# Performance work log

Measured on AMD Instinct MI355X. Metric: run time of the kernel, lower is better.

## Reference

```python
import jax, jax.numpy as jnp
import numpy as np

BETA = 0.9       # snn.Leaky(beta=0.9)
THRESH = 1.0     # snntorch default threshold, reset_mechanism='subtract'


def setup_inputs() -> dict:
    key = jax.random.key(0)
    ks = jax.random.split(key, 7)
    B = 16384
    return {
        "x":  jax.random.normal(ks[0], (B, 1700), dtype=jnp.float32),
        "W1": jax.random.normal(ks[1], (64, 1700), dtype=jnp.float32) * 0.02,
        "b1": jax.random.normal(ks[2], (64,), dtype=jnp.float32) * 0.02,
        "W2": jax.random.normal(ks[3], (32, 64), dtype=jnp.float32) * 0.1,
        "b2": jax.random.normal(ks[4], (32,), dtype=jnp.float32) * 0.1,
        "W3": jax.random.normal(ks[5], (2, 32), dtype=jnp.float32) * 0.1,
        "b3": jax.random.normal(ks[6], (2,), dtype=jnp.float32) * 0.1,
        "num_steps": 20,
    }


def _lif_step(mem, cur):
    # snntorch Leaky: reset (subtract) based on previous mem crossing threshold,
    # then leaky integration of the new input current.
    reset = (mem > THRESH).astype(mem.dtype)
    return BETA * mem + cur - reset * THRESH


def reference(x, W1, b1, W2, b2, W3, b3, num_steps):
    B = x.shape[0]
    # Dropout is identity in eval mode; x is constant across steps, so cur1 is
    # loop-invariant and computed once (same math as the original loop).
    cur1 = x @ W1.T + b1                         # [B, 64]

    def step(carry, _):
        mem1, mem2 = carry
        mem1 = _lif_step(mem1, cur1)             # [B, 64]
        cur2 = mem1 @ W2.T + b2                  # [B, 32]
        mem2 = _lif_step(mem2, cur2)             # [B, 32]
        return (mem1, mem2), None

    init = (jnp.zeros((B, 64), x.dtype), jnp.zeros((B, 32), x.dtype))
    (mem1, mem2), _ = jax.lax.scan(step, init, None, length=num_steps)
    return mem2 @ W3.T + b3                      # [B, 2]
```

## Files before the change

kernel.cpp:

```cpp
#include <hip/hip_runtime.h>
#include <hip/hip_bf16.h>

typedef float f32x4 __attribute__((ext_vector_type(4)));
typedef short bf16x8 __attribute__((ext_vector_type(8)));

#define MFMA16 __builtin_amdgcn_mfma_f32_16x16x32_bf16

static constexpr int KDIM = 1700;
static constexpr int NKT  = 54;
static constexpr float BETA = 0.9f;
static constexpr float THRESH = 1.0f;

__device__ __forceinline__ void split_bf(float f, short& hi, short& lo) {
    __hip_bfloat16 h = __float2bfloat16(f);
    float r = f - __bfloat162float(h);
    __hip_bfloat16 l = __float2bfloat16(r);
    hi = (short)__builtin_bit_cast(unsigned short, h);
    lo = (short)__builtin_bit_cast(unsigned short, l);
}

__device__ __forceinline__ void split8(f32x4 a, f32x4 b, bf16x8& hi, bf16x8& lo) {
    #pragma unroll
    for (int i = 0; i < 4; ++i) { short h, l; split_bf(a[i], h, l); hi[i] = h; lo[i] = l; }
    #pragma unroll
    for (int i = 0; i < 4; ++i) { short h, l; split_bf(b[i], h, l); hi[4 + i] = h; lo[4 + i] = l; }
}

__global__ void w1_relayout(const float* __restrict__ W1,
                            short* __restrict__ WTh, short* __restrict__ WTl) {
    const int g    = blockIdx.x * 256 + threadIdx.x;
    const int kt   = g >> 8;
    const int nt   = (g >> 6) & 3;
    const int lane = g & 63;
    const int n    = nt * 16 + (lane & 15);
    const int kb   = kt * 32 + (lane >> 4) * 8;
    bf16x8 vh, vl;
    #pragma unroll
    for (int i = 0; i < 8; ++i) {
        const int k = kb + i;
        const float v = (k < KDIM) ? W1[n * KDIM + k] : 0.f;
        short h, l; split_bf(v, h, l);
        vh[i] = h; vl[i] = l;
    }
    *(bf16x8*)(WTh + (size_t)g * 8) = vh;
    *(bf16x8*)(WTl + (size_t)g * 8) = vl;
}

__global__ __launch_bounds__(256, 2) void gemm1(
    const float* __restrict__ x,
    const short* __restrict__ WTh, const short* __restrict__ WTl,
    const float* __restrict__ b1, float* __restrict__ cur1)
{
    __shared__ float red[4][32][68];
    const int tid = threadIdx.x;
    const int wid = tid >> 6;
    const int lane = tid & 63;
    const int l15 = lane & 15;
    const int g4  = lane >> 4;
    const int kg  = g4 * 8;
    const int rowBase = blockIdx.x * 32;

    const int t0  = wid * 13 + (wid < 2 ? wid : 2);
    const int t1  = t0 + 14 - (wid >> 1);
    const int t1e = (wid == 3) ? 53 : t1;

    f32x4 acc[2][4] = {};
    const float* xr0 = x + (size_t)(rowBase + l15) * KDIM + kg;
    const float* xr1 = xr0 + (size_t)16 * KDIM;

    f32x4 p00 = *(const f32x4*)(xr0 + t0 * 32);
    f32x4 p01 = *(const f32x4*)(xr0 + t0 * 32 + 4);
    f32x4 p10 = *(const f32x4*)(xr1 + t0 * 32);
    f32x4 p11 = *(const f32x4*)(xr1 + t0 * 32 + 4);

    for (int t = t0; t < t1e; ++t) {
        f32x4 a00 = p00, a01 = p01, a10 = p10, a11 = p11;
        if (t + 1 < t1e) {
            p00 = *(const f32x4*)(xr0 + (t + 1) * 32);
            p01 = *(const f32x4*)(xr0 + (t + 1) * 32 + 4);
            p10 = *(const f32x4*)(xr1 + (t + 1) * 32);
            p11 = *(const f32x4*)(xr1 + (t + 1) * 32 + 4);
        }
        const short* wb = WTh + (size_t)t * 2048 + lane * 8;
        const short* wl = WTl + (size_t)t * 2048 + lane * 8;
        bf16x8 bh[4], bl[4];
        #pragma unroll
        for (int nt = 0; nt < 4; ++nt) {
            bh[nt] = *(const bf16x8*)(wb + nt * 512);
            bl[nt] = *(const bf16x8*)(wl + nt * 512);
        }
        bf16x8 ah0, al0, ah1, al1;
        split8(a00, a01, ah0, al0);
        split8(a10, a11, ah1, al1);
        #pragma unroll
        for (int nt = 0; nt < 4; ++nt) {
            acc[0][nt] = MFMA16(ah0, bh[nt], acc[0][nt], 0, 0, 0);
            acc[0][nt] = MFMA16(al0, bh[nt], acc[0][nt], 0, 0, 0);
            acc[0][nt] = MFMA16(ah0, bl[nt], acc[0][nt], 0, 0, 0);
            acc[1][nt] = MFMA16(ah1, bh[nt], acc[1][nt], 0, 0, 0);
            acc[1][nt] = MFMA16(al1, bh[nt], acc[1][nt], 0, 0, 0);
            acc[1][nt] = MFMA16(ah1, bl[nt], acc[1][nt], 0, 0, 0);
        }
    }
    if (wid == 3) {
        f32x4 a00 = {0,0,0,0}, a01 = {0,0,0,0}, a10 = {0,0,0,0}, a11 = {0,0,0,0};
        if (g4 == 0) {
            a00 = *(const f32x4*)(xr0 + 53 * 32);
            a10 = *(const f32x4*)(xr1 + 53 * 32);
        }
        const short* wb = WTh + (size_t)53 * 2048 + lane * 8;
        const short* wl = WTl + (size_t)53 * 2048 + lane * 8;
        bf16x8 bh[4], bl[4];
        #pragma unroll
        for (int nt = 0; nt < 4; ++nt) {
            bh[nt] = *(const bf16x8*)(wb + nt * 512);
            bl[nt] = *(const bf16x8*)(wl + nt * 512);
        }
        bf16x8 ah0, al0, ah1, al1;
        split8(a00, a01, ah0, al0);
        split8(a10, a11, ah1, al1);
        #pragma unroll
        for (int nt = 0; nt < 4; ++nt) {
            acc[0][nt] = MFMA16(ah0, bh[nt], acc[0][nt], 0, 0, 0);
            acc[0][nt] = MFMA16(al0, bh[nt], acc[0][nt], 0, 0, 0);
            acc[0][nt] = MFMA16(ah0, bl[nt], acc[0][nt], 0, 0, 0);
            acc[1][nt] = MFMA16(ah1, bh[nt], acc[1][nt], 0, 0, 0);
            acc[1][nt] = MFMA16(al1, bh[nt], acc[1][nt], 0, 0, 0);
            acc[1][nt] = MFMA16(ah1, bl[nt], acc[1][nt], 0, 0, 0);
        }
    }

    #pragma unroll
    for (int mt = 0; mt < 2; ++mt)
        #pragma unroll
        for (int nt = 0; nt < 4; ++nt)
            #pragma unroll
            for (int j = 0; j < 4; ++j)
                red[wid][mt * 16 + g4 * 4 + j][nt * 16 + l15] = acc[mt][nt][j];
    __syncthreads();

    const int rr  = tid >> 3;
    const int seg = tid & 7;
    f32x4 s0 = {0,0,0,0}, s1 = {0,0,0,0};
    #pragma unroll
    for (int p = 0; p < 4; ++p) {
        s0 += *(const f32x4*)&red[p][rr][seg * 8];
        s1 += *(const f32x4*)&red[p][rr][seg * 8 + 4];
    }
    s0 += *(const f32x4*)(b1 + seg * 8);
    s1 += *(const f32x4*)(b1 + seg * 8 + 4);
    float* cp = cur1 + (size_t)(rowBase + rr) * 64 + seg * 8;
    *(f32x4*)cp = s0;
    *(f32x4*)(cp + 4) = s1;
}

__global__ __launch_bounds__(256, 2) void recur(
    const float* __restrict__ cur1, const float* __restrict__ W2,
    const float* __restrict__ b2, const float* __restrict__ W3,
    const float* __restrict__ b3, const int* __restrict__ nsp,
    float* __restrict__ out)
{
    const int tid = threadIdx.x;
    const int wid = tid >> 6;
    const int lane = tid & 63;
    const int l15 = lane & 15;
    const int g4  = lane >> 4;
    const int kg  = g4 * 8;
    const int row = blockIdx.x * 64 + wid * 16 + l15;

    float c1[2][8];
    #pragma unroll
    for (int kt = 0; kt < 2; ++kt) {
        f32x4 u0 = *(const f32x4*)(cur1 + (size_t)row * 64 + kt * 32 + kg);
        f32x4 u1 = *(const f32x4*)(cur1 + (size_t)row * 64 + kt * 32 + kg + 4);
        #pragma unroll
        for (int i = 0; i < 4; ++i) { c1[kt][i] = u0[i]; c1[kt][4 + i] = u1[i]; }
    }

    bf16x8 W2hf[2][2], W2lf[2][2];
    #pragma unroll
    for (int rt = 0; rt < 2; ++rt)
        #pragma unroll
        for (int kt = 0; kt < 2; ++kt) {
            const float* wp = W2 + (rt * 16 + l15) * 64 + kt * 32 + kg;
            split8(*(const f32x4*)wp, *(const f32x4*)(wp + 4), W2hf[rt][kt], W2lf[rt][kt]);
        }

    float b2v[2][4], w3a[2][4], w3b[2][4];
    #pragma unroll
    for (int nt = 0; nt < 2; ++nt)
        #pragma unroll
        for (int j = 0; j < 4; ++j) {
            const int o = nt * 16 + g4 * 4 + j;
            b2v[nt][j] = b2[o];
            w3a[nt][j] = W3[o];
            w3b[nt][j] = W3[32 + o];
        }

    float m1[2][8] = {};
    float m2[2][4] = {};
    const int ns = nsp[0];
    for (int s = 0; s < ns; ++s) {
        bf16x8 mh[2], ml[2];
        #pragma unroll
        for (int kt = 0; kt < 2; ++kt)
            #pragma unroll
            for (int i = 0; i < 8; ++i) {
                float m = m1[kt][i];
                float rr = (m > THRESH) ? THRESH : 0.f;
                m = __builtin_fmaf(BETA, m, c1[kt][i] - rr);
                m1[kt][i] = m;
                short h, l; split_bf(m, h, l);
                mh[kt][i] = h; ml[kt][i] = l;
            }
        f32x4 a2[2][2] = {};
        #pragma unroll
        for (int rt = 0; rt < 2; ++rt)
            #pragma unroll
            for (int kt = 0; kt < 2; ++kt) {
                a2[rt][kt] = MFMA16(W2hf[rt][kt], mh[kt], a2[rt][kt], 0, 0, 0);
                a2[rt][kt] = MFMA16(W2lf[rt][kt], mh[kt], a2[rt][kt], 0, 0, 0);
                a2[rt][kt] = MFMA16(W2hf[rt][kt], ml[kt], a2[rt][kt], 0, 0, 0);
            }
        #pragma unroll
        for (int nt = 0; nt < 2; ++nt) {
            f32x4 c2 = a2[nt][0] + a2[nt][1];
            #pragma unroll
            for (int j = 0; j < 4; ++j) {
                float m = m2[nt][j];
                float rr = (m > THRESH) ? THRESH : 0.f;
                m2[nt][j] = __builtin_fmaf(BETA, m, c2[j] + b2v[nt][j] - rr);
            }
        }
    }

    float p0 = 0.f, p1 = 0.f;
    #pragma unroll
    for (int nt = 0; nt < 2; ++nt)
        #pragma unroll
        for (int j = 0; j < 4; ++j) {
            p0 = __builtin_fmaf(m2[nt][j], w3a[nt][j], p0);
            p1 = __builtin_fmaf(m2[nt][j], w3b[nt][j], p1);
        }
    p0 += __shfl_xor(p0, 16); p0 += __shfl_xor(p0, 32);
    p1 += __shfl_xor(p1, 16); p1 += __shfl_xor(p1, 32);
    if (lane < 16) {
        out[(size_t)row * 2 + 0] = p0 + b3[0];
        out[(size_t)row * 2 + 1] = p1 + b3[1];
    }
}

extern "C" void kernel_launch(void* const* d_in, const int* in_sizes, int n_in,
                              void* d_out, int out_size, void* d_ws, size_t ws_size,
                              hipStream_t stream) {
    const float* x  = (const float*)d_in[0];
    const float* W1 = (const float*)d_in[1];
    const float* b1 = (const float*)d_in[2];
    const float* W2 = (const float*)d_in[3];
    const float* b2 = (const float*)d_in[4];
    const float* W3 = (const float*)d_in[5];
    const float* b3 = (const float*)d_in[6];
    const int*   ns = (const int*)d_in[7];
    float* o = (float*)d_out;

    const int B = in_sizes[0] / KDIM;
    float* cur1 = (float*)d_ws;
    short* WTh  = (short*)((char*)d_ws + (size_t)B * 64 * 4);
    short* WTl  = WTh + (size_t)NKT * 2048;

    w1_relayout<<<NKT, 256, 0, stream>>>(W1, WTh, WTl);
    gemm1<<<B / 32, 256, 0, stream>>>(x, WTh, WTl, b1, cur1);
    recur<<<B / 64, 256, 0, stream>>>(cur1, W2, b2, W3, b3, ns, o);
}
```

Before: 44.51 us.

## Share W1 tiles via LDS with async global-to-LDS loads and 64-row blocks

Each gemm1 block now covers 64 rows instead of 32. The four waves split into two row halves times two K halves, and they stage the W1 hi/lo bf16 planes into double-buffered LDS with global_load_lds. Each wave then reads B fragments from LDS instead of global memory, which removes per-wave redundant weight loads and halves the reduction partners. The costs are a block-wide barrier on every K step, one block per CU from the launch bounds, and half as many blocks.

```diff
diff --git a/kernel.cpp b/kernel.cpp
--- a/kernel.cpp
+++ b/kernel.cpp
@@ -8,6 +8,7 @@
 
 static constexpr int KDIM = 1700;
 static constexpr int NKT  = 54;
+static constexpr int HTILES = 27;
 static constexpr float BETA = 0.9f;
 static constexpr float THRESH = 1.0f;
 
@@ -46,89 +47,93 @@
     *(bf16x8*)(WTl + (size_t)g * 8) = vl;
 }
 
-__global__ __launch_bounds__(256, 2) void gemm1(
+__device__ __forceinline__ void gll16(const short* src, const short* lds_dst) {
+    __builtin_amdgcn_global_load_lds(
+        (const __attribute__((address_space(1))) unsigned int*)src,
+        (__attribute__((address_space(3))) unsigned int*)lds_dst, 16, 0, 0);
+}
+
+__global__ __launch_bounds__(256, 1) void gemm1(
     const float* __restrict__ x,
     const short* __restrict__ WTh, const short* __restrict__ WTl,
     const float* __restrict__ b1, float* __restrict__ cur1)
 {
-    __shared__ float red[4][32][68];
-    const int tid = threadIdx.x;
-    const int wid = tid >> 6;
+    __shared__ __align__(1024) char smem[2 * 64 * 68 * 4];
+    short* ldsW = (short*)smem;
+    float (*red)[64][68] = (float (*)[64][68])smem;
+
+    const int tid  = threadIdx.x;
+    const int wid  = tid >> 6;
     const int lane = tid & 63;
-    const int l15 = lane & 15;
-    const int g4  = lane >> 4;
-    const int kg  = g4 * 8;
-    const int rowBase = blockIdx.x * 32;
-
-    const int t0  = wid * 13 + (wid < 2 ? wid : 2);
-    const int t1  = t0 + 14 - (wid >> 1);
-    const int t1e = (wid == 3) ? 53 : t1;
+    const int l15  = lane & 15;
+    const int g4   = lane >> 4;
+    const int kg   = g4 * 8;
+    const int kh   = wid & 1;
+    const int rh   = wid >> 1;
+    const int rowBase = blockIdx.x * 64;
+
+    const float* xr0 = x + (size_t)(rowBase + rh * 32 + l15) * KDIM + kg;
+    const float* xr1 = xr0 + (size_t)16 * KDIM;
+
+    const short* myPlane = (wid & 1) ? WTl : WTh;
+    const int    myTileOfs = (wid >> 1) ? HTILES : 0;
+
+    auto loadx = [&](int tile, f32x4& a00, f32x4& a01, f32x4& a10, f32x4& a11) {
+        if (tile < 53) {
+            a00 = *(const f32x4*)(xr0 + tile * 32);
+            a01 = *(const f32x4*)(xr0 + tile * 32 + 4);
+            a10 = *(const f32x4*)(xr1 + tile * 32);
+            a11 = *(const f32x4*)(xr1 + tile * 32 + 4);
+        } else {
+            a00 = a01 = a10 = a11 = (f32x4){0, 0, 0, 0};
+            if (g4 == 0) {
+                a00 = *(const f32x4*)(xr0 + 53 * 32);
+                a10 = *(const f32x4*)(xr1 + 53 * 32);
+            }
+        }
+    };
+    auto stage = [&](int buf, int s) {
+        const size_t gofs = (size_t)(myTileOfs + s) * 2048 + lane * 8;
+        const short* dst = ldsW + buf * 8192 + wid * 2048;
+        #pragma unroll
+        for (int i = 0; i < 4; ++i)
+            gll16(myPlane + gofs + i * 512, dst + i * 512);
+    };
+
+    f32x4 a00, a01, a10, a11;
+    loadx(kh * HTILES, a00, a01, a10, a11);
+    stage(0, 0);
+    __syncthreads();
 
     f32x4 acc[2][4] = {};
-    const float* xr0 = x + (size_t)(rowBase + l15) * KDIM + kg;
-    const float* xr1 = xr0 + (size_t)16 * KDIM;
-
-    f32x4 p00 = *(const f32x4*)(xr0 + t0 * 32);
-    f32x4 p01 = *(const f32x4*)(xr0 + t0 * 32 + 4);
-    f32x4 p10 = *(const f32x4*)(xr1 + t0 * 32);
-    f32x4 p11 = *(const f32x4*)(xr1 + t0 * 32 + 4);
-
-    for (int t = t0; t < t1e; ++t) {
-        f32x4 a00 = p00, a01 = p01, a10 = p10, a11 = p11;
-        if (t + 1 < t1e) {
-            p00 = *(const f32x4*)(xr0 + (t + 1) * 32);
-            p01 = *(const f32x4*)(xr0 + (t + 1) * 32 + 4);
-            p10 = *(const f32x4*)(xr1 + (t + 1) * 32);
-            p11 = *(const f32x4*)(xr1 + (t + 1) * 32 + 4);
-        }
-        const short* wb = WTh + (size_t)t * 2048 + lane * 8;
-        const short* wl = WTl + (size_t)t * 2048 + lane * 8;
-        bf16x8 bh[4], bl[4];
-        #pragma unroll
-        for (int nt = 0; nt < 4; ++nt) {
-            bh[nt] = *(const bf16x8*)(wb + nt * 512);
-            bl[nt] = *(const bf16x8*)(wl + nt * 512);
+    f32x4 p00, p01, p10, p11;
+    for (int s = 0; s < HTILES; ++s) {
+        const int buf = s & 1;
+        if (s + 1 < HTILES) {
+            loadx(kh * HTILES + s + 1, p00, p01, p10, p11);
+            stage(buf ^ 1, s + 1);
         }
         bf16x8 ah0, al0, ah1, al1;
         split8(a00, a01, ah0, al0);
         split8(a10, a11, ah1, al1);
+        const short* wb = ldsW + buf * 8192 + kh * 4096;
         #pragma unroll
         for (int nt = 0; nt < 4; ++nt) {
-            acc[0][nt] = MFMA16(ah0, bh[nt], acc[0][nt], 0, 0, 0);
-            acc[0][nt] = MFMA16(al0, bh[nt], acc[0][nt], 0, 0, 0);
-            acc[0][nt] = MFMA16(ah0, bl[nt], acc[0][nt], 0, 0, 0);
-            acc[1][nt] = MFMA16(ah1, bh[nt], acc[1][nt], 0, 0, 0);
-            acc[1][nt] = MFMA16(al1, bh[nt], acc[1][nt], 0, 0, 0);
-            acc[1][nt] = MFMA16(ah1, bl[nt], acc[1][nt], 0, 0, 0);
-        }
-    }
-    if (wid == 3) {
-        f32x4 a00 = {0,0,0,0}, a01 = {0,0,0,0}, a10 = {0,0,0,0}, a11 = {0,0,0,0};
-        if (g4 == 0) {
-            a00 = *(const f32x4*)(xr0 + 53 * 32);
-            a10 = *(const f32x4*)(xr1 + 53 * 32);
-        }
-        const short* wb = WTh + (size_t)53 * 2048 + lane * 8;
-        const short* wl = WTl + (size_t)53 * 2048 + lane * 8;
-        bf16x8 bh[4], bl[4];
-        #pragma unroll
-        for (int nt = 0; nt < 4; ++nt) {
-            bh[nt] = *(const bf16x8*)(wb + nt * 512);
-            bl[nt] = *(const bf16x8*)(wl + nt * 512);
-        }
-        bf16x8 ah0, al0, ah1, al1;
-        split8(a00, a01, ah0, al0);
-        split8(a10, a11, ah1, al1);
-        #pragma unroll
-        for (int nt = 0; nt < 4; ++nt) {
-            acc[0][nt] = MFMA16(ah0, bh[nt], acc[0][nt], 0, 0, 0);
-            acc[0][nt] = MFMA16(al0, bh[nt], acc[0][nt], 0, 0, 0);
-            acc[0][nt] = MFMA16(ah0, bl[nt], acc[0][nt], 0, 0, 0);
-            acc[1][nt] = MFMA16(ah1, bh[nt], acc[1][nt], 0, 0, 0);
-            acc[1][nt] = MFMA16(al1, bh[nt], acc[1][nt], 0, 0, 0);
-            acc[1][nt] = MFMA16(ah1, bl[nt], acc[1][nt], 0, 0, 0);
-        }
-    }
+            bf16x8 bh = *(const bf16x8*)(wb + nt * 512 + lane * 8);
+            bf16x8 bl = *(const bf16x8*)(wb + 2048 + nt * 512 + lane * 8);
+            acc[0][nt] = MFMA16(ah0, bh, acc[0][nt], 0, 0, 0);
+            acc[0][nt] = MFMA16(al0, bh, acc[0][nt], 0, 0, 0);
+            acc[0][nt] = MFMA16(ah0, bl, acc[0][nt], 0, 0, 0);
+            acc[1][nt] = MFMA16(ah1, bh, acc[1][nt], 0, 0, 0);
+            acc[1][nt] = MFMA16(al1, bh, acc[1][nt], 0, 0, 0);
+            acc[1][nt] = MFMA16(ah1, bl, acc[1][nt], 0, 0, 0);
+        }
+        if (s + 1 < HTILES) {
+            __syncthreads();
+            a00 = p00; a01 = p01; a10 = p10; a11 = p11;
+        }
+    }
+    __syncthreads();
 
     #pragma unroll
     for (int mt = 0; mt < 2; ++mt)
@@ -136,22 +141,24 @@
         for (int nt = 0; nt < 4; ++nt)
             #pragma unroll
             for (int j = 0; j < 4; ++j)
-                red[wid][mt * 16 + g4 * 4 + j][nt * 16 + l15] = acc[mt][nt][j];
+                red[kh][rh * 32 + mt * 16 + g4 * 4 + j][nt * 16 + l15] = acc[mt][nt][j];
     __syncthreads();
 
-    const int rr  = tid >> 3;
-    const int seg = tid & 7;
-    f32x4 s0 = {0,0,0,0}, s1 = {0,0,0,0};
-    #pragma unroll
-    for (int p = 0; p < 4; ++p) {
-        s0 += *(const f32x4*)&red[p][rr][seg * 8];
-        s1 += *(const f32x4*)&red[p][rr][seg * 8 + 4];
-    }
-    s0 += *(const f32x4*)(b1 + seg * 8);
-    s1 += *(const f32x4*)(b1 + seg * 8 + 4);
-    float* cp = cur1 + (size_t)(rowBase + rr) * 64 + seg * 8;
-    *(f32x4*)cp = s0;
-    *(f32x4*)(cp + 4) = s1;
+    #pragma unroll
+    for (int it = 0; it < 2; ++it) {
+        const int task = tid + it * 256;
+        const int row = task >> 3;
+        const int seg = task & 7;
+        f32x4 s0 = *(const f32x4*)&red[0][row][seg * 8]
+                 + *(const f32x4*)&red[1][row][seg * 8]
+                 + *(const f32x4*)(b1 + seg * 8);
+        f32x4 s1 = *(const f32x4*)&red[0][row][seg * 8 + 4]
+                 + *(const f32x4*)&red[1][row][seg * 8 + 4]
+                 + *(const f32x4*)(b1 + seg * 8 + 4);
+        float* cp = cur1 + (size_t)(rowBase + row) * 64 + seg * 8;
+        *(f32x4*)cp = s0;
+        *(f32x4*)(cp + 4) = s1;
+    }
 }
 
 __global__ __launch_bounds__(256, 2) void recur(
@@ -269,6 +276,6 @@
     short* WTl  = WTh + (size_t)NKT * 2048;
 
     w1_relayout<<<NKT, 256, 0, stream>>>(W1, WTh, WTl);
-    gemm1<<<B / 32, 256, 0, stream>>>(x, WTh, WTl, b1, cur1);
+    gemm1<<<B / 64, 256, 0, stream>>>(x, WTh, WTl, b1, cur1);
     recur<<<B / 64, 256, 0, stream>>>(cur1, W2, b2, W3, b3, ns, o);
 }
```

New measurement: 53.14 us. 1.19x slower.

## Fuse layer-1 GEMM with LIF recurrence, keeping cur1 in shared memory

Applied to the files above, without the earlier changes.

Merges the gemm1 and recur kernels into one kernel. After the cross-wave reduction, cur1 stays in LDS and is read by two of the four waves, which run the 20-step recurrence, so the cur1 round-trip through global memory and one kernel launch go away. The LIF reset is also rewritten as a select between precomputed (cur - thresh) and cur values, removing a subtract per step. The cost is that half the waves sit idle during the serial recurrence while still holding their registers and LDS.

```diff
diff --git a/kernel.cpp b/kernel.cpp
--- a/kernel.cpp
+++ b/kernel.cpp
@@ -46,10 +46,13 @@
     *(bf16x8*)(WTl + (size_t)g * 8) = vl;
 }
 
-__global__ __launch_bounds__(256, 2) void gemm1(
+__global__ __launch_bounds__(256, 2) void snn_fused(
     const float* __restrict__ x,
     const short* __restrict__ WTh, const short* __restrict__ WTl,
-    const float* __restrict__ b1, float* __restrict__ cur1)
+    const float* __restrict__ b1, const float* __restrict__ W2,
+    const float* __restrict__ b2, const float* __restrict__ W3,
+    const float* __restrict__ b3, const int* __restrict__ nsp,
+    float* __restrict__ out)
 {
     __shared__ float red[4][32][68];
     const int tid = threadIdx.x;
@@ -60,121 +63,115 @@
     const int kg  = g4 * 8;
     const int rowBase = blockIdx.x * 32;
 
-    const int t0  = wid * 13 + (wid < 2 ? wid : 2);
-    const int t1  = t0 + 14 - (wid >> 1);
-    const int t1e = (wid == 3) ? 53 : t1;
-
-    f32x4 acc[2][4] = {};
-    const float* xr0 = x + (size_t)(rowBase + l15) * KDIM + kg;
-    const float* xr1 = xr0 + (size_t)16 * KDIM;
-
-    f32x4 p00 = *(const f32x4*)(xr0 + t0 * 32);
-    f32x4 p01 = *(const f32x4*)(xr0 + t0 * 32 + 4);
-    f32x4 p10 = *(const f32x4*)(xr1 + t0 * 32);
-    f32x4 p11 = *(const f32x4*)(xr1 + t0 * 32 + 4);
-
-    for (int t = t0; t < t1e; ++t) {
-        f32x4 a00 = p00, a01 = p01, a10 = p10, a11 = p11;
-        if (t + 1 < t1e) {
-            p00 = *(const f32x4*)(xr0 + (t + 1) * 32);
-            p01 = *(const f32x4*)(xr0 + (t + 1) * 32 + 4);
-            p10 = *(const f32x4*)(xr1 + (t + 1) * 32);
-            p11 = *(const f32x4*)(xr1 + (t + 1) * 32 + 4);
-        }
-        const short* wb = WTh + (size_t)t * 2048 + lane * 8;
-        const short* wl = WTl + (size_t)t * 2048 + lane * 8;
-        bf16x8 bh[4], bl[4];
-        #pragma unroll
-        for (int nt = 0; nt < 4; ++nt) {
-            bh[nt] = *(const bf16x8*)(wb + nt * 512);
-            bl[nt] = *(const bf16x8*)(wl + nt * 512);
-        }
-        bf16x8 ah0, al0, ah1, al1;
-        split8(a00, a01, ah0, al0);
-        split8(a10, a11, ah1, al1);
-        #pragma unroll
-        for (int nt = 0; nt < 4; ++nt) {
-            acc[0][nt] = MFMA16(ah0, bh[nt], acc[0][nt], 0, 0, 0);
-            acc[0][nt] = MFMA16(al0, bh[nt], acc[0][nt], 0, 0, 0);
-            acc[0][nt] = MFMA16(ah0, bl[nt], acc[0][nt], 0, 0, 0);
-            acc[1][nt] = MFMA16(ah1, bh[nt], acc[1][nt], 0, 0, 0);
-            acc[1][nt] = MFMA16(al1, bh[nt], acc[1][nt], 0, 0, 0);
-            acc[1][nt] = MFMA16(ah1, bl[nt], acc[1][nt], 0, 0, 0);
-        }
-    }
-    if (wid == 3) {
-        f32x4 a00 = {0,0,0,0}, a01 = {0,0,0,0}, a10 = {0,0,0,0}, a11 = {0,0,0,0};
-        if (g4 == 0) {
-            a00 = *(const f32x4*)(xr0 + 53 * 32);
-            a10 = *(const f32x4*)(xr1 + 53 * 32);
-        }
-        const short* wb = WTh + (size_t)53 * 2048 + lane * 8;
-        const short* wl = WTl + (size_t)53 * 2048 + lane * 8;
-        bf16x8 bh[4], bl[4];
-        #pragma unroll
-        for (int nt = 0; nt < 4; ++nt) {
-            bh[nt] = *(const bf16x8*)(wb + nt * 512);
-            bl[nt] = *(const bf16x8*)(wl + nt * 512);
-        }
-        bf16x8 ah0, al0, ah1, al1;
-        split8(a00, a01, ah0, al0);
-        split8(a10, a11, ah1, al1);
-        #pragma unroll
-        for (int nt = 0; nt < 4; ++nt) {
-            acc[0][nt] = MFMA16(ah0, bh[nt], acc[0][nt], 0, 0, 0);
-            acc[0][nt] = MFMA16(al0, bh[nt], acc[0][nt], 0, 0, 0);
-            acc[0][nt] = MFMA16(ah0, bl[nt], acc[0][nt], 0, 0, 0);
-            acc[1][nt] = MFMA16(ah1, bh[nt], acc[1][nt], 0, 0, 0);
-            acc[1][nt] = MFMA16(al1, bh[nt], acc[1][nt], 0, 0, 0);
-            acc[1][nt] = MFMA16(ah1, bl[nt], acc[1][nt], 0, 0, 0);
-        }
-    }
-
-    #pragma unroll
-    for (int mt = 0; mt < 2; ++mt)
-        #pragma unroll
-        for (int nt = 0; nt < 4; ++nt)
-            #pragma unroll
-            for (int j = 0; j < 4; ++j)
-                red[wid][mt * 16 + g4 * 4 + j][nt * 16 + l15] = acc[mt][nt][j];
+    {
+        const int t0  = wid * 13 + (wid < 2 ? wid : 2);
+        const int t1  = t0 + 14 - (wid >> 1);
+        const int t1e = (wid == 3) ? 53 : t1;
+
+        const float* xr0 = x + (size_t)(rowBase + l15) * KDIM + kg;
+        const float* xr1 = xr0 + (size_t)16 * KDIM;
+
+        f32x4 acc[2][4] = {};
+        f32x4 p00 = *(const f32x4*)(xr0 + t0 * 32);
+        f32x4 p01 = *(const f32x4*)(xr0 + t0 * 32 + 4);
+        f32x4 p10 = *(const f32x4*)(xr1 + t0 * 32);
+        f32x4 p11 = *(const f32x4*)(xr1 + t0 * 32 + 4);
+
+        for (int t = t0; t < t1e; ++t) {
+            f32x4 a00 = p00, a01 = p01, a10 = p10, a11 = p11;
+            if (t + 1 < t1e) {
+                p00 = *(const f32x4*)(xr0 + (t + 1) * 32);
+                p01 = *(const f32x4*)(xr0 + (t + 1) * 32 + 4);
+                p10 = *(const f32x4*)(xr1 + (t + 1) * 32);
+                p11 = *(const f32x4*)(xr1 + (t + 1) * 32 + 4);
+            }
+            const short* wb = WTh + (size_t)t * 2048 + lane * 8;
+            const short* wl = WTl + (size_t)t * 2048 + lane * 8;
+            bf16x8 bh[4], bl[4];
+            #pragma unroll
+            for (int nt = 0; nt < 4; ++nt) {
+                bh[nt] = *(const bf16x8*)(wb + nt * 512);
+                bl[nt] = *(const bf16x8*)(wl + nt * 512);
+            }
+            bf16x8 ah0, al0, ah1, al1;
+            split8(a00, a01, ah0, al0);
+            split8(a10, a11, ah1, al1);
+            #pragma unroll
+            for (int nt = 0; nt < 4; ++nt) {
+                acc[0][nt] = MFMA16(ah0, bh[nt], acc[0][nt], 0, 0, 0);
+                acc[0][nt] = MFMA16(al0, bh[nt], acc[0][nt], 0, 0, 0);
+                acc[0][nt] = MFMA16(ah0, bl[nt], acc[0][nt], 0, 0, 0);
+                acc[1][nt] = MFMA16(ah1, bh[nt], acc[1][nt], 0, 0, 0);
+                acc[1][nt] = MFMA16(al1, bh[nt], acc[1][nt], 0, 0, 0);
+                acc[1][nt] = MFMA16(ah1, bl[nt], acc[1][nt], 0, 0, 0);
+            }
+        }
+        if (wid == 3) {
+            f32x4 a00 = {0,0,0,0}, a01 = {0,0,0,0}, a10 = {0,0,0,0}, a11 = {0,0,0,0};
+            if (g4 == 0) {
+                a00 = *(const f32x4*)(xr0 + 53 * 32);
+                a10 = *(const f32x4*)(xr1 + 53 * 32);
+            }
+            const short* wb = WTh + (size_t)53 * 2048 + lane * 8;
+            const short* wl = WTl + (size_t)53 * 2048 + lane * 8;
+            bf16x8 bh[4], bl[4];
+            #pragma unroll
+            for (int nt = 0; nt < 4; ++nt) {
+                bh[nt] = *(const bf16x8*)(wb + nt * 512);
+                bl[nt] = *(const bf16x8*)(wl + nt * 512);
+            }
+            bf16x8 ah0, al0, ah1, al1;
+            split8(a00, a01, ah0, al0);
+            split8(a10, a11, ah1, al1);
+            #pragma unroll
+            for (int nt = 0; nt < 4; ++nt) {
+                acc[0][nt] = MFMA16(ah0, bh[nt], acc[0][nt], 0, 0, 0);
+                acc[0][nt] = MFMA16(al0, bh[nt], acc[0][nt], 0, 0, 0);
+                acc[0][nt] = MFMA16(ah0, bl[nt], acc[0][nt], 0, 0, 0);
+                acc[1][nt] = MFMA16(ah1, bh[nt], acc[1][nt], 0, 0, 0);
+                acc[1][nt] = MFMA16(al1, bh[nt], acc[1][nt], 0, 0, 0);
+                acc[1][nt] = MFMA16(ah1, bl[nt], acc[1][nt], 0, 0, 0);
+            }
+        }
+
+        #pragma unroll
+        for (int mt = 0; mt < 2; ++mt)
+            #pragma unroll
+            for (int nt = 0; nt < 4; ++nt)
+                #pragma unroll
+                for (int j = 0; j < 4; ++j)
+                    red[wid][mt * 16 + g4 * 4 + j][nt * 16 + l15] = acc[mt][nt][j];
+    }
     __syncthreads();
 
-    const int rr  = tid >> 3;
-    const int seg = tid & 7;
-    f32x4 s0 = {0,0,0,0}, s1 = {0,0,0,0};
-    #pragma unroll
-    for (int p = 0; p < 4; ++p) {
-        s0 += *(const f32x4*)&red[p][rr][seg * 8];
-        s1 += *(const f32x4*)&red[p][rr][seg * 8 + 4];
-    }
-    s0 += *(const f32x4*)(b1 + seg * 8);
-    s1 += *(const f32x4*)(b1 + seg * 8 + 4);
-    float* cp = cur1 + (size_t)(rowBase + rr) * 64 + seg * 8;
-    *(f32x4*)cp = s0;
-    *(f32x4*)(cp + 4) = s1;
-}
-
-__global__ __launch_bounds__(256, 2) void recur(
-    const float* __restrict__ cur1, const float* __restrict__ W2,
-    const float* __restrict__ b2, const float* __restrict__ W3,
-    const float* __restrict__ b3, const int* __restrict__ nsp,
-    float* __restrict__ out)
-{
-    const int tid = threadIdx.x;
-    const int wid = tid >> 6;
-    const int lane = tid & 63;
-    const int l15 = lane & 15;
-    const int g4  = lane >> 4;
-    const int kg  = g4 * 8;
-    const int row = blockIdx.x * 64 + wid * 16 + l15;
-
-    float c1[2][8];
+    {
+        const int rr  = tid >> 3;
+        const int seg = tid & 7;
+        f32x4 s0 = *(const f32x4*)(b1 + seg * 8);
+        f32x4 s1 = *(const f32x4*)(b1 + seg * 8 + 4);
+        #pragma unroll
+        for (int p = 0; p < 4; ++p) {
+            s0 += *(const f32x4*)&red[p][rr][seg * 8];
+            s1 += *(const f32x4*)&red[p][rr][seg * 8 + 4];
+        }
+        *(f32x4*)&red[0][rr][seg * 8]     = s0;
+        *(f32x4*)&red[0][rr][seg * 8 + 4] = s1;
+    }
+    __syncthreads();
+    if (wid >= 2) return;
+
+    const int lrow = wid * 16 + l15;
+
+    float c1[2][8], c1m1[2][8];
     #pragma unroll
     for (int kt = 0; kt < 2; ++kt) {
-        f32x4 u0 = *(const f32x4*)(cur1 + (size_t)row * 64 + kt * 32 + kg);
-        f32x4 u1 = *(const f32x4*)(cur1 + (size_t)row * 64 + kt * 32 + kg + 4);
-        #pragma unroll
-        for (int i = 0; i < 4; ++i) { c1[kt][i] = u0[i]; c1[kt][4 + i] = u1[i]; }
+        f32x4 u0 = *(const f32x4*)&red[0][lrow][kt * 32 + kg];
+        f32x4 u1 = *(const f32x4*)&red[0][lrow][kt * 32 + kg + 4];
+        #pragma unroll
+        for (int i = 0; i < 4; ++i) {
+            c1[kt][i] = u0[i];     c1[kt][4 + i] = u1[i];
+            c1m1[kt][i] = u0[i] - THRESH; c1m1[kt][4 + i] = u1[i] - THRESH;
+        }
     }
 
     bf16x8 W2hf[2][2], W2lf[2][2];
@@ -186,13 +183,14 @@
             split8(*(const f32x4*)wp, *(const f32x4*)(wp + 4), W2hf[rt][kt], W2lf[rt][kt]);
         }
 
-    float b2v[2][4], w3a[2][4], w3b[2][4];
+    float b2v[2][4], b2m1[2][4], w3a[2][4], w3b[2][4];
     #pragma unroll
     for (int nt = 0; nt < 2; ++nt)
         #pragma unroll
         for (int j = 0; j < 4; ++j) {
             const int o = nt * 16 + g4 * 4 + j;
-            b2v[nt][j] = b2[o];
+            b2v[nt][j]  = b2[o];
+            b2m1[nt][j] = b2[o] - THRESH;
             w3a[nt][j] = W3[o];
             w3b[nt][j] = W3[32 + o];
         }
@@ -207,8 +205,7 @@
             #pragma unroll
             for (int i = 0; i < 8; ++i) {
                 float m = m1[kt][i];
-                float rr = (m > THRESH) ? THRESH : 0.f;
-                m = __builtin_fmaf(BETA, m, c1[kt][i] - rr);
+                m = __builtin_fmaf(BETA, m, (m > THRESH) ? c1m1[kt][i] : c1[kt][i]);
                 m1[kt][i] = m;
                 short h, l; split_bf(m, h, l);
                 mh[kt][i] = h; ml[kt][i] = l;
@@ -228,8 +225,8 @@
             #pragma unroll
             for (int j = 0; j < 4; ++j) {
                 float m = m2[nt][j];
-                float rr = (m > THRESH) ? THRESH : 0.f;
-                m2[nt][j] = __builtin_fmaf(BETA, m, c2[j] + b2v[nt][j] - rr);
+                m2[nt][j] = __builtin_fmaf(
+                    BETA, m, c2[j] + ((m > THRESH) ? b2m1[nt][j] : b2v[nt][j]));
             }
         }
     }
@@ -245,8 +242,9 @@
     p0 += __shfl_xor(p0, 16); p0 += __shfl_xor(p0, 32);
     p1 += __shfl_xor(p1, 16); p1 += __shfl_xor(p1, 32);
     if (lane < 16) {
-        out[(size_t)row * 2 + 0] = p0 + b3[0];
-        out[(size_t)row * 2 + 1] = p1 + b3[1];
+        const size_t row = rowBase + lrow;
+        out[row * 2 + 0] = p0 + b3[0];
+        out[row * 2 + 1] = p1 + b3[1];
     }
 }
 
@@ -264,11 +262,9 @@
     float* o = (float*)d_out;
 
     const int B = in_sizes[0] / KDIM;
-    float* cur1 = (float*)d_ws;
-    short* WTh  = (short*)((char*)d_ws + (size_t)B * 64 * 4);
+    short* WTh  = (short*)d_ws;
     short* WTl  = WTh + (size_t)NKT * 2048;
 
     w1_relayout<<<NKT, 256, 0, stream>>>(W1, WTh, WTl);
-    gemm1<<<B / 32, 256, 0, stream>>>(x, WTh, WTl, b1, cur1);
-    recur<<<B / 64, 256, 0, stream>>>(cur1, W2, b2, W3, b3, ns, o);
-}
+    snn_fused<<<B / 32, 256, 0, stream>>>(x, WTh, WTl, b1, W2, b2, W3, b3, ns, o);
+}
```

Measured after the change: 44.07 us. Within noise of the previous version (-1.0%).
